# Kernel tuning notes

Measured on AMD Instinct MI355X. Metric: run time of the kernel, lower is better.

Reference implementation:

```python
import jax, jax.numpy as jnp
import numpy as np
from jax.scipy.special import logsumexp

B, L, S, C = 8, 2048, 2048, 256
ITERS = 20

def setup_inputs() -> dict:
    key = jax.random.key(0)
    k0, k1 = jax.random.split(key)
    feat_c0 = jax.random.normal(k0, (B, L, C), dtype=jnp.float32)
    feat_c1 = jax.random.normal(k1, (B, S, C), dtype=jnp.float32)
    bin_score = jnp.ones((), dtype=jnp.float32)  # init_bin_score = 1.0
    return {"feat_c0": feat_c0, "feat_c1": feat_c1, "bin_score": bin_score}

def _uniform_prior(b, m, n):
    # build_uniform_prior: norm = -log(m+n); log_mu/[log_nu] over augmented rows/cols
    fm, fn = jnp.float32(m), jnp.float32(n)
    norm = -jnp.log(fm + fn)
    log_mu = jnp.concatenate([jnp.full((m,), norm, jnp.float32), (jnp.log(fn) + norm)[None]])
    log_nu = jnp.concatenate([jnp.full((n,), norm, jnp.float32), (jnp.log(fm) + norm)[None]])
    log_mu = jnp.broadcast_to(log_mu[None], (b, m + 1))
    log_nu = jnp.broadcast_to(log_nu[None], (b, n + 1))
    return log_mu, log_nu, norm

def _log_sinkhorn(Z, log_mu, log_nu, iters):
    u0 = jnp.zeros_like(log_mu)
    v0 = jnp.zeros_like(log_nu)
    def body(carry, _):
        u, v = carry
        u = log_mu - logsumexp(Z + v[:, None, :], axis=2)  # [B, M+1]
        v = log_nu - logsumexp(Z + u[:, :, None], axis=1)  # [B, N+1]
        return (u, v), None
    (u, v), _ = jax.lax.scan(body, (u0, v0), None, length=iters)
    return Z + u[:, :, None] + v[:, None, :]

def reference(feat_c0, feat_c1, bin_score):
    b, m, n = feat_c0.shape[0], feat_c0.shape[1], feat_c1.shape[1]
    scores = jnp.einsum('blc,bsc->bls', feat_c0, feat_c1)  # [B, M, N]
    # augment with dustbin row/col
    bins0 = jnp.broadcast_to(bin_score, (b, m, 1))
    bins1 = jnp.broadcast_to(bin_score, (b, 1, n))
    alpha = jnp.broadcast_to(bin_score, (b, 1, 1))
    Zin = jnp.concatenate([
        jnp.concatenate([scores, bins0], axis=-1),
        jnp.concatenate([bins1, alpha], axis=-1),
    ], axis=1)  # [B, M+1, N+1]
    log_mu, log_nu, norm = _uniform_prior(b, m, n)
    Z = _log_sinkhorn(Zin, log_mu, log_nu, ITERS)
    return Z - norm
```

## Files before the change

kernel.cpp:

```cpp
#include <hip/hip_runtime.h>

#define Bn 8
#define Mn 2048
#define Nn 2048
#define Cn 256
#define Np1 2049
#define Mp1 2049
#define UVS 2056
#define SINK_ITERS 20
#define NORM   (-8.3177661667193428f)
#define LOGBIN (-0.6931471805599453f)

typedef __bf16 v8bf __attribute__((ext_vector_type(8)));
typedef float  v4f  __attribute__((ext_vector_type(4)));
typedef unsigned short v8u __attribute__((ext_vector_type(8)));

__device__ __forceinline__ float bf2f(unsigned short h){
  return __uint_as_float(((unsigned)h) << 16);
}
__device__ __forceinline__ unsigned short f2bf(float f){
  unsigned u = __float_as_uint(f);
  return (unsigned short)((u + 0x7FFFu + ((u >> 16) & 1u)) >> 16);
}
__device__ __forceinline__ float ldS(const float* p){ return *p; }
__device__ __forceinline__ float ldS(const unsigned short* p){ return bf2f(*p); }
__device__ __forceinline__ void  stS(float* p, float x){ *p = x; }
__device__ __forceinline__ void  stS(unsigned short* p, float x){ *p = f2bf(x); }

__device__ __forceinline__ void ons(float x, float& m, float& s){
  if (x <= m) { s += __expf(x - m); }
  else        { s = s * __expf(m - x) + 1.0f; m = x; }
}
__device__ __forceinline__ void comb(float& m, float& s, float m2, float s2){
  if (m2 <= m) { s += s2 * __expf(m2 - m); }
  else         { s = s * __expf(m - m2) + s2; m = m2; }
}

template<typename ST>
__global__ void __launch_bounds__(256) gemm_k(
    const float* __restrict__ A, const float* __restrict__ Bm,
    ST* __restrict__ S, long srow, long sbatch)
{
  int wid  = (blockIdx.x * 256 + threadIdx.x) >> 6;
  int lane = threadIdx.x & 63;
  int b  = wid >> 10;
  int tt = wid & 1023;
  int i0 = (tt >> 5) << 6;
  int j0 = (tt & 31) << 6;
  int ln = lane & 15, qd = lane >> 4;
  const float* Ab = A  + (size_t)b * Mn * Cn;
  const float* Bb = Bm + (size_t)b * Nn * Cn;

  v4f acc[4][4];
  #pragma unroll
  for (int r = 0; r < 4; ++r)
    #pragma unroll
    for (int c = 0; c < 4; ++c)
      #pragma unroll
      for (int e = 0; e < 4; ++e) acc[r][c][e] = 0.0f;

  #pragma unroll
  for (int k0 = 0; k0 < Cn; k0 += 32){
    int kk = k0 + qd * 8;
    v8bf af[4], bfr[4];
    #pragma unroll
    for (int r = 0; r < 4; ++r){
      const float* p = Ab + (size_t)(i0 + r*16 + ln) * Cn + kk;
      v4f lo = *(const v4f*)p, hi = *(const v4f*)(p + 4);
      #pragma unroll
      for (int e = 0; e < 4; ++e){ af[r][e] = (__bf16)lo[e]; af[r][e+4] = (__bf16)hi[e]; }
    }
    #pragma unroll
    for (int c = 0; c < 4; ++c){
      const float* p = Bb + (size_t)(j0 + c*16 + ln) * Cn + kk;
      v4f lo = *(const v4f*)p, hi = *(const v4f*)(p + 4);
      #pragma unroll
      for (int e = 0; e < 4; ++e){ bfr[c][e] = (__bf16)lo[e]; bfr[c][e+4] = (__bf16)hi[e]; }
    }
    #pragma unroll
    for (int r = 0; r < 4; ++r)
      #pragma unroll
      for (int c = 0; c < 4; ++c)
        acc[r][c] = __builtin_amdgcn_mfma_f32_16x16x32_bf16(af[r], bfr[c], acc[r][c], 0, 0, 0);
  }

  ST* Sb = S + (size_t)b * sbatch;
  #pragma unroll
  for (int r = 0; r < 4; ++r){
    #pragma unroll
    for (int e = 0; e < 4; ++e){
      int row = i0 + r*16 + qd*4 + e;
      #pragma unroll
      for (int c = 0; c < 4; ++c)
        stS(Sb + (size_t)row * srow + (j0 + c*16 + ln), acc[r][c][e]);
    }
  }
}

__global__ void __launch_bounds__(256) row_pass_t(
    const unsigned short* __restrict__ S, const float* __restrict__ vin,
    float* __restrict__ uout, const float* __restrict__ binp)
{
  int b = blockIdx.y, t = threadIdx.x;
  const float* vb = vin + (size_t)b * UVS;
  __shared__ float red[8];
  if (blockIdx.x < Mn / 4){
    int lane = t & 63;
    int i = blockIdx.x * 4 + (t >> 6);
    const unsigned short* Sr = S + ((size_t)b * Mn + i) * Nn;
    float x[32];
    #pragma unroll
    for (int q = 0; q < 4; ++q){
      int j0 = q * 512 + lane * 8;
      v8u sv = *(const v8u*)(Sr + j0);
      v4f va = *(const v4f*)(vb + j0);
      v4f vc = *(const v4f*)(vb + j0 + 4);
      #pragma unroll
      for (int c = 0; c < 4; ++c){
        x[q*8 + c]     = bf2f(sv[c])   + va[c];
        x[q*8 + 4 + c] = bf2f(sv[c+4]) + vc[c];
      }
    }
    float mx[16];
    #pragma unroll
    for (int k = 0; k < 16; ++k) mx[k] = fmaxf(x[2*k], x[2*k+1]);
    #pragma unroll
    for (int k = 0; k < 8; ++k) mx[k] = fmaxf(mx[k], mx[k+8]);
    #pragma unroll
    for (int k = 0; k < 4; ++k) mx[k] = fmaxf(mx[k], mx[k+4]);
    float m = fmaxf(fmaxf(mx[0], mx[1]), fmaxf(mx[2], mx[3]));
    #pragma unroll
    for (int off = 32; off > 0; off >>= 1) m = fmaxf(m, __shfl_xor(m, off));
    float s0 = 0.f, s1 = 0.f, s2 = 0.f, s3 = 0.f;
    #pragma unroll
    for (int k = 0; k < 8; ++k){
      s0 += __expf(x[4*k]     - m);
      s1 += __expf(x[4*k + 1] - m);
      s2 += __expf(x[4*k + 2] - m);
      s3 += __expf(x[4*k + 3] - m);
    }
    float s = (s0 + s1) + (s2 + s3);
    #pragma unroll
    for (int off = 32; off > 0; off >>= 1) s += __shfl_xor(s, off);
    if (lane == 0){
      float M = m, Ss = s;
      comb(M, Ss, binp[0] + vb[Nn], 1.0f);
      uout[(size_t)b * UVS + i] = NORM - (M + __logf(Ss));
    }
  } else {
    float x[9];
    #pragma unroll
    for (int k = 0; k < 9; ++k){
      int j = t + k * 256;
      x[k] = (j <= Nn) ? vb[j] : -3.0e38f;
    }
    float m = x[0];
    #pragma unroll
    for (int k = 1; k < 9; ++k) m = fmaxf(m, x[k]);
    #pragma unroll
    for (int off = 32; off > 0; off >>= 1) m = fmaxf(m, __shfl_down(m, off));
    int w = t >> 6;
    if ((t & 63) == 0) red[w] = m;
    __syncthreads();
    float M = fmaxf(fmaxf(red[0], red[1]), fmaxf(red[2], red[3]));
    float s = 0.0f;
    #pragma unroll
    for (int k = 0; k < 9; ++k) s += __expf(x[k] - M);
    #pragma unroll
    for (int off = 32; off > 0; off >>= 1) s += __shfl_down(s, off);
    __syncthreads();
    if ((t & 63) == 0) red[w] = s;
    __syncthreads();
    if (t == 0){
      float Ss = red[0] + red[1] + red[2] + red[3];
      uout[(size_t)b * UVS + Mn] = LOGBIN - (binp[0] + M + __logf(Ss));
    }
  }
}


__global__ void __launch_bounds__(256) row_pass_v(
    const unsigned short* __restrict__ S, const float* __restrict__ v,
    float* __restrict__ u, const float* __restrict__ binp)
{
  int i = blockIdx.x, b = blockIdx.y, t = threadIdx.x;
  const float* vb = v + (size_t)b * UVS;
  float x[9];
  int K;
  if (i < Mn){
    const unsigned short* Sr = S + ((size_t)b * Mn + i) * Nn;
    int j0 = t * 8;
    v8u sv = *(const v8u*)(Sr + j0);
    v4f va = *(const v4f*)(vb + j0);
    v4f vc = *(const v4f*)(vb + j0 + 4);
    #pragma unroll
    for (int c = 0; c < 4; ++c){ x[c] = bf2f(sv[c]) + va[c]; x[c+4] = bf2f(sv[c+4]) + vc[c]; }
    K = 8;
  } else {
    #pragma unroll
    for (int k = 0; k < 9; ++k){
      int j = t + k * 256;
      x[k] = (j <= Nn) ? vb[j] : -3.0e38f;
    }
    K = 9;
  }
  float m = x[0];
  #pragma unroll
  for (int k = 1; k < 9; ++k) if (k < K) m = fmaxf(m, x[k]);
  #pragma unroll
  for (int off = 32; off > 0; off >>= 1) m = fmaxf(m, __shfl_down(m, off));
  __shared__ float red[8];
  int w = t >> 6;
  if ((t & 63) == 0) red[w] = m;
  __syncthreads();
  float M = fmaxf(fmaxf(red[0], red[1]), fmaxf(red[2], red[3]));
  float s = 0.0f;
  #pragma unroll
  for (int k = 0; k < 9; ++k) if (k < K) s += __expf(x[k] - M);
  #pragma unroll
  for (int off = 32; off > 0; off >>= 1) s += __shfl_down(s, off);
  __syncthreads();
  if ((t & 63) == 0) red[w] = s;
  __syncthreads();
  if (t == 0){
    float Ss = red[0] + red[1] + red[2] + red[3];
    float bin = binp[0];
    if (i < Mn){
      comb(M, Ss, bin + vb[Nn], 1.0f);
      u[(size_t)b * UVS + i] = NORM - (M + __logf(Ss));
    } else {
      u[(size_t)b * UVS + Mn] = LOGBIN - (bin + M + __logf(Ss));
    }
  }
}

__global__ void __launch_bounds__(256) col_pass_v(
    const unsigned short* __restrict__ S, const float* __restrict__ u,
    float* __restrict__ v, const float* __restrict__ binp)
{
  int blk = blockIdx.x, b = blockIdx.y, t = threadIdx.x;
  const float* ub = u + (size_t)b * UVS;
  __shared__ float lm[32][65];
  __shared__ float ls[32][65];
  __shared__ float red[16];
  if (blk < Nn / 64){
    int tx = t & 7, ty = t >> 3;
    int j0 = blk * 64 + tx * 8;
    const unsigned short* Sb = S + (size_t)b * Mn * Nn;
    float m[8], s[8];
    #pragma unroll
    for (int c = 0; c < 8; ++c){ m[c] = -3.0e38f; s[c] = 0.0f; }
    for (int i = ty; i < Mn; i += 32){
      v8u sv = *(const v8u*)(Sb + (size_t)i * Nn + j0);
      float ui = ub[i];
      #pragma unroll
      for (int c = 0; c < 8; ++c){
        float x  = bf2f(sv[c]) + ui;
        float mn = fmaxf(m[c], x);
        s[c] = s[c] * __expf(m[c] - mn) + __expf(x - mn);
        m[c] = mn;
      }
    }
    #pragma unroll
    for (int c = 0; c < 8; ++c){ lm[ty][tx*8 + c] = m[c]; ls[ty][tx*8 + c] = s[c]; }
    __syncthreads();
    if (t < 64){
      float M = -3.0e38f, Ss = 0.0f;
      #pragma unroll 4
      for (int rg = 0; rg < 32; ++rg) comb(M, Ss, lm[rg][t], ls[rg][t]);
      float bin = binp[0];
      comb(M, Ss, bin + ub[Mn], 1.0f);
      v[(size_t)b * UVS + blk * 64 + t] = NORM - (M + __logf(Ss));
    }
  } else {
    float x[9];
    #pragma unroll
    for (int k = 0; k < 9; ++k){
      int j = t + k * 256;
      x[k] = (j <= Mn) ? ub[j] : -3.0e38f;
    }
    float m = x[0];
    #pragma unroll
    for (int k = 1; k < 9; ++k) m = fmaxf(m, x[k]);
    #pragma unroll
    for (int off = 32; off > 0; off >>= 1) m = fmaxf(m, __shfl_down(m, off));
    int w = t >> 6;
    if ((t & 63) == 0) red[w] = m;
    __syncthreads();
    float M = fmaxf(fmaxf(red[0], red[1]), fmaxf(red[2], red[3]));
    float s = 0.0f;
    #pragma unroll
    for (int k = 0; k < 9; ++k) s += __expf(x[k] - M);
    #pragma unroll
    for (int off = 32; off > 0; off >>= 1) s += __shfl_down(s, off);
    __syncthreads();
    if ((t & 63) == 0) red[w] = s;
    __syncthreads();
    if (t == 0){
      float Ss = red[0] + red[1] + red[2] + red[3];
      float bin = binp[0];
      v[(size_t)b * UVS + Nn] = LOGBIN - (bin + M + __logf(Ss));
    }
  }
}

__global__ void __launch_bounds__(256) final_v(
    const unsigned short* __restrict__ S, float* __restrict__ out,
    const float* __restrict__ u, const float* __restrict__ v,
    const float* __restrict__ binp)
{
  int i = blockIdx.x, b = blockIdx.y, t = threadIdx.x;
  float bin = binp[0];
  const float* vb = v + (size_t)b * UVS;
  float ui = u[(size_t)b * UVS + i];
  float* ob = out + ((size_t)b * Mp1 + i) * Np1;
  if (i < Mn){
    const unsigned short* Sr = S + ((size_t)b * Mn + i) * Nn;
    int j0 = t * 8;
    v8u sv = *(const v8u*)(Sr + j0);
    v4f va = *(const v4f*)(vb + j0);
    v4f vc = *(const v4f*)(vb + j0 + 4);
    #pragma unroll
    for (int c = 0; c < 4; ++c) ob[j0 + c]     = bf2f(sv[c])   + ui + va[c] - NORM;
    #pragma unroll
    for (int c = 0; c < 4; ++c) ob[j0 + 4 + c] = bf2f(sv[c+4]) + ui + vc[c] - NORM;
    if (t == 0) ob[Nn] = bin + ui + vb[Nn] - NORM;
  } else {
    for (int j = t; j <= Nn; j += 256) ob[j] = bin + ui + vb[j] - NORM;
  }
}


template<typename ST>
__global__ void __launch_bounds__(256) row_pass(
    const ST* __restrict__ S, long srow, long sbatch,
    const float* __restrict__ v, float* __restrict__ u,
    const float* __restrict__ binp)
{
  int i = blockIdx.x, b = blockIdx.y, t = threadIdx.x;
  const float* vb = v + (size_t)b * UVS;
  float m = -3.0e38f, s = 0.0f;
  if (i < Mn){
    const ST* Sr = S + (size_t)b * sbatch + (size_t)i * srow;
    #pragma unroll
    for (int jj = 0; jj < Nn / 256; ++jj){
      int j = jj * 256 + t;
      ons(ldS(Sr + j) + vb[j], m, s);
    }
  } else {
    for (int j = t; j <= Nn; j += 256) ons(vb[j], m, s);
  }
  #pragma unroll
  for (int off = 32; off > 0; off >>= 1){
    float m2 = __shfl_down(m, off);
    float s2 = __shfl_down(s, off);
    comb(m, s, m2, s2);
  }
  __shared__ float sm[4], ss[4];
  int w = t >> 6;
  if ((t & 63) == 0){ sm[w] = m; ss[w] = s; }
  __syncthreads();
  if (t == 0){
    #pragma unroll
    for (int w2 = 1; w2 < 4; ++w2) comb(m, s, sm[w2], ss[w2]);
    float bin = binp[0];
    if (i < Mn){
      comb(m, s, bin + vb[Nn], 1.0f);
      u[(size_t)b * UVS + i] = NORM - (m + __logf(s));
    } else {
      u[(size_t)b * UVS + Mn] = LOGBIN - (bin + m + __logf(s));
    }
  }
}

template<typename ST>
__global__ void __launch_bounds__(1024) col_pass(
    const ST* __restrict__ S, long srow, long sbatch,
    const float* __restrict__ u, float* __restrict__ v,
    const float* __restrict__ binp)
{
  int jt = blockIdx.x, b = blockIdx.y, t = threadIdx.x;
  const float* ub = u + (size_t)b * UVS;
  __shared__ float sm[16][64];
  __shared__ float ss[16][64];
  if (jt < Nn / 64){
    int c = t & 63, rg = t >> 6;
    int j = jt * 64 + c;
    const ST* Sc = S + (size_t)b * sbatch + j;
    float m = -3.0e38f, s = 0.0f;
    #pragma unroll 8
    for (int i = rg; i < Mn; i += 16)
      ons(ldS(Sc + (size_t)i * srow) + ub[i], m, s);
    sm[rg][c] = m; ss[rg][c] = s;
    __syncthreads();
    if (rg == 0){
      #pragma unroll
      for (int r = 1; r < 16; ++r) comb(m, s, sm[r][c], ss[r][c]);
      float bin = binp[0];
      comb(m, s, bin + ub[Mn], 1.0f);
      v[(size_t)b * UVS + j] = NORM - (m + __logf(s));
    }
  } else {
    float m = -3.0e38f, s = 0.0f;
    for (int i = t; i <= Mn; i += 1024) ons(ub[i], m, s);
    #pragma unroll
    for (int off = 32; off > 0; off >>= 1){
      float m2 = __shfl_down(m, off);
      float s2 = __shfl_down(s, off);
      comb(m, s, m2, s2);
    }
    int w = t >> 6;
    if ((t & 63) == 0){ sm[0][w] = m; ss[0][w] = s; }
    __syncthreads();
    if (t == 0){
      #pragma unroll
      for (int w2 = 1; w2 < 16; ++w2) comb(m, s, sm[0][w2], ss[0][w2]);
      float bin = binp[0];
      v[(size_t)b * UVS + Nn] = LOGBIN - (bin + m + __logf(s));
    }
  }
}

template<typename ST>
__global__ void __launch_bounds__(256) final_k(
    const ST* __restrict__ S, long srow, long sbatch,
    float* __restrict__ out, const float* __restrict__ u,
    const float* __restrict__ v, const float* __restrict__ binp)
{
  int i = blockIdx.x, b = blockIdx.y, t = threadIdx.x;
  float bin = binp[0];
  float ui = u[(size_t)b * UVS + i];
  const float* vb = v + (size_t)b * UVS;
  float* ob = out + ((size_t)b * Mp1 + i) * Np1;
  if (i < Mn){
    const ST* Sr = S + (size_t)b * sbatch + (size_t)i * srow;
    for (int j = t; j < Nn; j += 256)
      ob[j] = ldS(Sr + j) + ui + vb[j] - NORM;
    if (t == 0) ob[Nn] = bin + ui + vb[Nn] - NORM;
  } else {
    for (int j = t; j <= Nn; j += 256)
      ob[j] = bin + ui + vb[j] - NORM;
  }
}

__global__ void zero_uv(float* uv){
  int t = blockIdx.x * 256 + threadIdx.x;
  if (t < 2 * Bn * UVS) uv[t] = 0.0f;
}

extern "C" void kernel_launch(void* const* d_in, const int* in_sizes, int n_in,
                              void* d_out, int out_size, void* d_ws, size_t ws_size,
                              hipStream_t stream)
{
  const float* A    = (const float*)d_in[0];
  const float* Bm   = (const float*)d_in[1];
  const float* binp = (const float*)d_in[2];
  float* out = (float*)d_out;

  const size_t S_bytes  = (size_t)Bn * Mn * Nn * 2;
  const size_t uv_bytes = (size_t)2 * Bn * UVS * 4;
  bool useT = ws_size >= 2 * S_bytes + uv_bytes;
  bool useW = ws_size >= S_bytes + uv_bytes;

  float* u;
  unsigned short* Sw  = nullptr;
  unsigned short* STw = nullptr;
  if (useT){
    Sw  = (unsigned short*)d_ws;
    STw = (unsigned short*)((char*)d_ws + S_bytes);
    u   = (float*)((char*)d_ws + 2 * S_bytes);
  } else if (useW){
    Sw = (unsigned short*)d_ws;
    u  = (float*)((char*)d_ws + S_bytes);
  } else {
    u  = (float*)d_ws;
  }
  float* v = u + (size_t)Bn * UVS;

  zero_uv<<<(2 * Bn * UVS + 255) / 256, 256, 0, stream>>>(u);

  if (useT){
    gemm_k<unsigned short><<<(Bn * 32 * 32) / 4, 256, 0, stream>>>(A, Bm, Sw,  Nn, (long)Mn * Nn);
    gemm_k<unsigned short><<<(Bn * 32 * 32) / 4, 256, 0, stream>>>(Bm, A, STw, Mn, (long)Mn * Nn);
    for (int it = 0; it < SINK_ITERS; ++it){
      row_pass_t<<<dim3(Mn / 4 + 1, Bn), 256, 0, stream>>>(Sw,  v, u, binp);
      row_pass_t<<<dim3(Nn / 4 + 1, Bn), 256, 0, stream>>>(STw, u, v, binp);
    }
    final_v<<<dim3(Mp1, Bn), 256, 0, stream>>>(Sw, out, u, v, binp);
  } else if (useW){
    gemm_k<unsigned short><<<(Bn * 32 * 32) / 4, 256, 0, stream>>>(A, Bm, Sw, Nn, (long)Mn * Nn);
    for (int it = 0; it < SINK_ITERS; ++it){
      row_pass_v<<<dim3(Mp1, Bn), 256, 0, stream>>>(Sw, v, u, binp);
      col_pass_v<<<dim3(Nn / 64 + 1, Bn), 256, 0, stream>>>(Sw, u, v, binp);
    }
    final_v<<<dim3(Mp1, Bn), 256, 0, stream>>>(Sw, out, u, v, binp);
  } else {
    const long srow = Np1, sbatch = (long)Mp1 * Np1;
    gemm_k<float><<<(Bn * 32 * 32) / 4, 256, 0, stream>>>(A, Bm, out, srow, sbatch);
    for (int it = 0; it < SINK_ITERS; ++it){
      row_pass<float><<<dim3(Mp1, Bn), 256, 0, stream>>>(out, srow, sbatch, v, u, binp);
      col_pass<float><<<dim3(Nn / 64 + 1, Bn), 1024, 0, stream>>>(out, srow, sbatch, u, v, binp);
    }
    final_k<float><<<dim3(Mp1, Bn), 256, 0, stream>>>(out, srow, sbatch, out, u, v, binp);
  }
}
```

Before: 896.3 us.

## Add base-2 log-domain Sinkhorn path with precomputed row maxima and bf16 GEMM inputs

Adds a new path that converts the fp32 features to bf16 once, runs a bf16 MFMA GEMM that stores scores pre-scaled by log2(e), and precomputes per-row maxima of S and S^T. Each Sinkhorn pass then uses a single-pass log-sum-exp: it takes the row max plus the max of v as the shift and sums with exp2, avoiding the online max/rescale logic. The final output is converted back from base 2 with a multiply by ln2. This needs extra workspace for the bf16 inputs and the row max arrays. The looser max bound risks losing precision in the sums.

```diff
diff --git a/kernel.cpp b/kernel.cpp
--- a/kernel.cpp
+++ b/kernel.cpp
@@ -10,6 +10,14 @@
 #define SINK_ITERS 20
 #define NORM   (-8.3177661667193428f)
 #define LOGBIN (-0.6931471805599453f)
+#define LOG2E  (1.4426950408889634f)
+#define LN2    (0.6931471805599453f)
+#define NORM2  (-12.0f)
+#define LOGBIN2 (-1.0f)
+#define PNORM  (8.3177661667193428f)
+
+#define EXP2(x) __builtin_amdgcn_exp2f(x)
+#define LOG2(x) __builtin_amdgcn_logf(x)
 
 typedef __bf16 v8bf __attribute__((ext_vector_type(8)));
 typedef float  v4f  __attribute__((ext_vector_type(4)));
@@ -34,6 +42,200 @@
 __device__ __forceinline__ void comb(float& m, float& s, float m2, float s2){
   if (m2 <= m) { s += s2 * __expf(m2 - m); }
   else         { s = s * __expf(m - m2) + s2; m = m2; }
+}
+
+__global__ void __launch_bounds__(256) conv_k(
+    const float* __restrict__ in, unsigned short* __restrict__ out, float scale)
+{
+  size_t idx = (size_t)blockIdx.x * 256 + threadIdx.x;
+  const float* p = in + idx * 8;
+  v4f a = *(const v4f*)p;
+  v4f c = *(const v4f*)(p + 4);
+  v8u o;
+  #pragma unroll
+  for (int e = 0; e < 4; ++e){ o[e] = f2bf(a[e] * scale); o[e+4] = f2bf(c[e] * scale); }
+  *(v8u*)(out + idx * 8) = o;
+}
+
+__global__ void __launch_bounds__(256) gemm_b(
+    const unsigned short* __restrict__ A, const unsigned short* __restrict__ Bm,
+    unsigned short* __restrict__ S, long srow)
+{
+  int wid  = (blockIdx.x * 256 + threadIdx.x) >> 6;
+  int lane = threadIdx.x & 63;
+  int b  = wid >> 10;
+  int tt = wid & 1023;
+  int i0 = (tt >> 5) << 6;
+  int j0 = (tt & 31) << 6;
+  int ln = lane & 15, qd = lane >> 4;
+  const unsigned short* Ab = A  + (size_t)b * Mn * Cn;
+  const unsigned short* Bb = Bm + (size_t)b * Nn * Cn;
+
+  v4f acc[4][4];
+  #pragma unroll
+  for (int r = 0; r < 4; ++r)
+    #pragma unroll
+    for (int c = 0; c < 4; ++c)
+      #pragma unroll
+      for (int e = 0; e < 4; ++e) acc[r][c][e] = 0.0f;
+
+  #pragma unroll
+  for (int k0 = 0; k0 < Cn; k0 += 32){
+    int kk = k0 + qd * 8;
+    v8bf af[4], bfr[4];
+    #pragma unroll
+    for (int r = 0; r < 4; ++r)
+      af[r] = *(const v8bf*)(const void*)(Ab + (size_t)(i0 + r*16 + ln) * Cn + kk);
+    #pragma unroll
+    for (int c = 0; c < 4; ++c)
+      bfr[c] = *(const v8bf*)(const void*)(Bb + (size_t)(j0 + c*16 + ln) * Cn + kk);
+    #pragma unroll
+    for (int r = 0; r < 4; ++r)
+      #pragma unroll
+      for (int c = 0; c < 4; ++c)
+        acc[r][c] = __builtin_amdgcn_mfma_f32_16x16x32_bf16(af[r], bfr[c], acc[r][c], 0, 0, 0);
+  }
+
+  unsigned short* Sb = S + (size_t)b * Mn * Nn;
+  #pragma unroll
+  for (int r = 0; r < 4; ++r){
+    #pragma unroll
+    for (int e = 0; e < 4; ++e){
+      int row = i0 + r*16 + qd*4 + e;
+      #pragma unroll
+      for (int c = 0; c < 4; ++c)
+        Sb[(size_t)row * srow + (j0 + c*16 + ln)] = f2bf(acc[r][c][e] * LOG2E);
+    }
+  }
+}
+
+__global__ void __launch_bounds__(256) rmax_k(
+    const unsigned short* __restrict__ S, float* __restrict__ rmax)
+{
+  int b = blockIdx.y, lane = threadIdx.x & 63;
+  int i = blockIdx.x * 4 + (threadIdx.x >> 6);
+  const unsigned short* Sr = S + ((size_t)b * Mn + i) * Nn;
+  float m = -3.0e38f;
+  #pragma unroll
+  for (int q = 0; q < 4; ++q){
+    v8u sv = *(const v8u*)(Sr + q * 512 + lane * 8);
+    #pragma unroll
+    for (int c = 0; c < 8; ++c) m = fmaxf(m, bf2f(sv[c]));
+  }
+  #pragma unroll
+  for (int off = 32; off > 0; off >>= 1) m = fmaxf(m, __shfl_xor(m, off));
+  if (lane == 0) rmax[(size_t)b * UVS + i] = m;
+}
+
+__global__ void __launch_bounds__(256) pass3_k(
+    const unsigned short* __restrict__ S, const float* __restrict__ vin,
+    float* __restrict__ uout, const float* __restrict__ rmax,
+    const float* __restrict__ binp)
+{
+  int b = blockIdx.y, t = threadIdx.x;
+  const float* vb = vin + (size_t)b * UVS;
+  __shared__ float red[8];
+  if (blockIdx.x < Mn / 4){
+    int lane = t & 63;
+    int i = blockIdx.x * 4 + (t >> 6);
+    const unsigned short* Sr = S + ((size_t)b * Mn + i) * Nn;
+    v4f va[8];
+    #pragma unroll
+    for (int q = 0; q < 4; ++q){
+      int j0 = q * 512 + lane * 8;
+      va[2*q]   = *(const v4f*)(vb + j0);
+      va[2*q+1] = *(const v4f*)(vb + j0 + 4);
+    }
+    float mv = va[0][0];
+    #pragma unroll
+    for (int h = 0; h < 8; ++h)
+      #pragma unroll
+      for (int e = 0; e < 4; ++e) mv = fmaxf(mv, va[h][e]);
+    #pragma unroll
+    for (int off = 32; off > 0; off >>= 1) mv = fmaxf(mv, __shfl_xor(mv, off));
+    float bin2 = binp[0] * LOG2E;
+    float vN = vb[Nn];
+    float shift = fmaxf(rmax[(size_t)b * UVS + i] + mv, bin2 + vN);
+    #pragma unroll
+    for (int h = 0; h < 8; ++h)
+      #pragma unroll
+      for (int e = 0; e < 4; ++e) va[h][e] -= shift;
+    float s0 = 0.f, s1 = 0.f, s2 = 0.f, s3 = 0.f;
+    #pragma unroll
+    for (int q = 0; q < 4; ++q){
+      v8u sv = *(const v8u*)(Sr + q * 512 + lane * 8);
+      s0 += EXP2(bf2f(sv[0]) + va[2*q][0]);
+      s1 += EXP2(bf2f(sv[1]) + va[2*q][1]);
+      s2 += EXP2(bf2f(sv[2]) + va[2*q][2]);
+      s3 += EXP2(bf2f(sv[3]) + va[2*q][3]);
+      s0 += EXP2(bf2f(sv[4]) + va[2*q+1][0]);
+      s1 += EXP2(bf2f(sv[5]) + va[2*q+1][1]);
+      s2 += EXP2(bf2f(sv[6]) + va[2*q+1][2]);
+      s3 += EXP2(bf2f(sv[7]) + va[2*q+1][3]);
+    }
+    float s = (s0 + s1) + (s2 + s3);
+    #pragma unroll
+    for (int off = 32; off > 0; off >>= 1) s += __shfl_xor(s, off);
+    if (lane == 0){
+      s += EXP2(bin2 + vN - shift);
+      uout[(size_t)b * UVS + i] = NORM2 - (shift + LOG2(s));
+    }
+  } else {
+    float x[9];
+    #pragma unroll
+    for (int k = 0; k < 9; ++k){
+      int j = t + k * 256;
+      x[k] = (j <= Nn) ? vb[j] : -3.0e38f;
+    }
+    float m = x[0];
+    #pragma unroll
+    for (int k = 1; k < 9; ++k) m = fmaxf(m, x[k]);
+    #pragma unroll
+    for (int off = 32; off > 0; off >>= 1) m = fmaxf(m, __shfl_down(m, off));
+    int w = t >> 6;
+    if ((t & 63) == 0) red[w] = m;
+    __syncthreads();
+    float M = fmaxf(fmaxf(red[0], red[1]), fmaxf(red[2], red[3]));
+    float s = 0.0f;
+    #pragma unroll
+    for (int k = 0; k < 9; ++k) s += EXP2(x[k] - M);
+    #pragma unroll
+    for (int off = 32; off > 0; off >>= 1) s += __shfl_down(s, off);
+    __syncthreads();
+    if ((t & 63) == 0) red[w] = s;
+    __syncthreads();
+    if (t == 0){
+      float Ss = red[0] + red[1] + red[2] + red[3];
+      float bin2 = binp[0] * LOG2E;
+      uout[(size_t)b * UVS + Mn] = LOGBIN2 - (bin2 + M + LOG2(Ss));
+    }
+  }
+}
+
+__global__ void __launch_bounds__(256) final2_k(
+    const unsigned short* __restrict__ S, float* __restrict__ out,
+    const float* __restrict__ u, const float* __restrict__ v,
+    const float* __restrict__ binp)
+{
+  int i = blockIdx.x, b = blockIdx.y, t = threadIdx.x;
+  float bin2 = binp[0] * LOG2E;
+  const float* vb = v + (size_t)b * UVS;
+  float ui = u[(size_t)b * UVS + i];
+  float* ob = out + ((size_t)b * Mp1 + i) * Np1;
+  if (i < Mn){
+    const unsigned short* Sr = S + ((size_t)b * Mn + i) * Nn;
+    int j0 = t * 8;
+    v8u sv = *(const v8u*)(Sr + j0);
+    v4f va = *(const v4f*)(vb + j0);
+    v4f vc = *(const v4f*)(vb + j0 + 4);
+    #pragma unroll
+    for (int c = 0; c < 4; ++c) ob[j0 + c]     = (bf2f(sv[c])   + ui + va[c]) * LN2 + PNORM;
+    #pragma unroll
+    for (int c = 0; c < 4; ++c) ob[j0 + 4 + c] = (bf2f(sv[c+4]) + ui + vc[c]) * LN2 + PNORM;
+    if (t == 0) ob[Nn] = (bin2 + ui + vb[Nn]) * LN2 + PNORM;
+  } else {
+    for (int j = t; j <= Nn; j += 256) ob[j] = (bin2 + ui + vb[j]) * LN2 + PNORM;
+  }
 }
 
 template<typename ST>
@@ -177,7 +379,6 @@
     }
   }
 }
-
 
 __global__ void __launch_bounds__(256) row_pass_v(
     const unsigned short* __restrict__ S, const float* __restrict__ v,
@@ -329,7 +530,6 @@
     for (int j = t; j <= Nn; j += 256) ob[j] = bin + ui + vb[j] - NORM;
   }
 }
-
 
 template<typename ST>
 __global__ void __launch_bounds__(256) row_pass(
@@ -458,14 +658,24 @@
   float* out = (float*)d_out;
 
   const size_t S_bytes  = (size_t)Bn * Mn * Nn * 2;
-  const size_t uv_bytes = (size_t)2 * Bn * UVS * 4;
-  bool useT = ws_size >= 2 * S_bytes + uv_bytes;
-  bool useW = ws_size >= S_bytes + uv_bytes;
+  const size_t AB_bytes = (size_t)Bn * Mn * Cn * 2;
+  const size_t uv_bytes = (size_t)4 * Bn * UVS * 4;
+  bool useT2 = ws_size >= 2 * S_bytes + 2 * AB_bytes + uv_bytes;
+  bool useT  = ws_size >= 2 * S_bytes + 2 * (size_t)Bn * UVS * 4;
+  bool useW  = ws_size >= S_bytes + 2 * (size_t)Bn * UVS * 4;
 
   float* u;
   unsigned short* Sw  = nullptr;
   unsigned short* STw = nullptr;
-  if (useT){
+  unsigned short* Abf = nullptr;
+  unsigned short* Bbf = nullptr;
+  if (useT2){
+    Sw  = (unsigned short*)d_ws;
+    STw = (unsigned short*)((char*)d_ws + S_bytes);
+    Abf = (unsigned short*)((char*)d_ws + 2 * S_bytes);
+    Bbf = (unsigned short*)((char*)d_ws + 2 * S_bytes + AB_bytes);
+    u   = (float*)((char*)d_ws + 2 * S_bytes + 2 * AB_bytes);
+  } else if (useT){
     Sw  = (unsigned short*)d_ws;
     STw = (unsigned short*)((char*)d_ws + S_bytes);
     u   = (float*)((char*)d_ws + 2 * S_bytes);
@@ -479,7 +689,22 @@
 
   zero_uv<<<(2 * Bn * UVS + 255) / 256, 256, 0, stream>>>(u);
 
-  if (useT){
+  if (useT2){
+    float* rmaxS = v + (size_t)Bn * UVS;
+    float* rmaxT = rmaxS + (size_t)Bn * UVS;
+    const int cgrid = (Bn * Mn * Cn / 8) / 256;
+    conv_k<<<cgrid, 256, 0, stream>>>(A,  Abf, 1.0f);
+    conv_k<<<cgrid, 256, 0, stream>>>(Bm, Bbf, 1.0f);
+    gemm_b<<<(Bn * 32 * 32) / 4, 256, 0, stream>>>(Abf, Bbf, Sw,  Nn);
+    gemm_b<<<(Bn * 32 * 32) / 4, 256, 0, stream>>>(Bbf, Abf, STw, Mn);
+    rmax_k<<<dim3(Mn / 4, Bn), 256, 0, stream>>>(Sw,  rmaxS);
+    rmax_k<<<dim3(Nn / 4, Bn), 256, 0, stream>>>(STw, rmaxT);
+    for (int it = 0; it < SINK_ITERS; ++it){
+      pass3_k<<<dim3(Mn / 4 + 1, Bn), 256, 0, stream>>>(Sw,  v, u, rmaxS, binp);
+      pass3_k<<<dim3(Nn / 4 + 1, Bn), 256, 0, stream>>>(STw, u, v, rmaxT, binp);
+    }
+    final2_k<<<dim3(Mp1, Bn), 256, 0, stream>>>(Sw, out, u, v, binp);
+  } else if (useT){
     gemm_k<unsigned short><<<(Bn * 32 * 32) / 4, 256, 0, stream>>>(A, Bm, Sw,  Nn, (long)Mn * Nn);
     gemm_k<unsigned short><<<(Bn * 32 * 32) / 4, 256, 0, stream>>>(Bm, A, STw, Mn, (long)Mn * Nn);
     for (int it = 0; it < SINK_ITERS; ++it){
```

New measurement: 793.4 us. -11.5%, faster.
